# Kernel tuning notes

Hardware: AMD Instinct MI355X
Metric: run time of the kernel (lower is better)

The kernel has to match this reference:

```python
import jax, jax.numpy as jnp
import numpy as np

K_SIZE = 5


def _extract_patches(x, k):
    """x: [n, b, h, w, c] -> [n, b, h, w, k*k, c] with zero SAME padding.

    Matches tf.image.extract_patches row-major patch ordering with channels
    fastest, as consumed by the Reshape((H, W, k*k, Ci)) in the original.
    """
    p = k // 2
    n, b, h, w, c = x.shape
    xp = jnp.pad(x, ((0, 0), (0, 0), (p, p), (p, p), (0, 0)))
    shifts = [xp[:, :, i:i + h, j:j + w, :] for i in range(k) for j in range(k)]
    return jnp.stack(shifts, axis=4)


def setup_inputs() -> dict:
    key = jax.random.key(0)
    k1, k2, k3, k4 = jax.random.split(key, 4)
    B, H, W, C = 4, 128, 128, 64
    heads, Ci = 4, 16  # intermediate_dim=64, head_num=4
    main = jax.random.normal(k1, (B, H, W, C), jnp.float32)
    ref = jax.random.normal(k2, (B, H, W, C), jnp.float32)
    he_std = np.sqrt(2.0 / C).astype(np.float32)  # he_normal, fan_in=C (1x1 conv)
    w_main = jax.random.normal(k3, (heads, C, Ci), jnp.float32) * he_std
    w_ref = jax.random.normal(k4, (heads, C, Ci), jnp.float32) * he_std
    return {"main": main, "ref": ref, "w_main": w_main, "w_ref": w_ref}


def reference(main, ref, w_main, w_ref):
    # per-head 1x1 convs (no bias): [n,b,h,w,d]
    q = jnp.einsum('bhwc,ncd->nbhwd', main, w_main)
    r = jnp.einsum('bhwc,ncd->nbhwd', ref, w_ref)
    patches = _extract_patches(r, K_SIZE)          # [n,b,h,w,k*k,d]
    attn = jnp.einsum('nbhwd,nbhwkd->nbhwk', q, patches)
    attn = jax.nn.softmax(attn, axis=-1)           # softmax over k*k neighbors
    return jnp.mean(attn, axis=0)                  # average over heads -> [b,h,w,k*k]
```

## Files before the change

kernel.cpp:

```cpp
#include <hip/hip_runtime.h>
#include <hip/hip_bf16.h>

typedef _Float16 f16;
typedef f16 f16x2 __attribute__((ext_vector_type(2)));
typedef f16 f16x4 __attribute__((ext_vector_type(4)));
typedef f16 f16x8 __attribute__((ext_vector_type(8)));
typedef float f32x4 __attribute__((ext_vector_type(4)));

constexpr int B_  = 4;
constexpr int H_  = 128;
constexpr int W_  = 128;
constexpr int C_  = 64;
constexpr int NH_ = 4;
constexpr int D_  = 16;
constexpr int KK_ = 25;

constexpr int TW_  = 8, TH_ = 8;
constexpr int HWID = 12, HHEI = 12;
constexpr int NPX  = HHEI * HWID;
constexpr int MOFF  = NPX * 64 * 2;
constexpr int MSOFF = 27648;
constexpr int SMEM  = 31744;
constexpr int PSTRIDE = KK_ + 2;
constexpr int PSLAB   = 64 * PSTRIDE;

#if __has_builtin(__builtin_amdgcn_fdot2)
#define FDOT2(a, b, c) __builtin_amdgcn_fdot2((a), (b), (c), false)
#else
#define FDOT2(a, b, c) fmaf((float)(a)[1], (float)(b)[1], fmaf((float)(a)[0], (float)(b)[0], (c)))
#endif

__device__ __forceinline__ int div12(int x) { return (x * 171) >> 11; }

__global__ __launch_bounds__(512, 8) void rl8mh8(
    const float* __restrict__ mainp, const float* __restrict__ refp,
    const float* __restrict__ wmain, const float* __restrict__ wref,
    float* __restrict__ out)
{
    __shared__ __align__(16) unsigned char smraw[SMEM];
    f16*    abuf  = (f16*)smraw;
    f16*    mabuf = (f16*)(smraw + MOFF);
    float*  xbuf  = (float*)smraw;
    float2* msbuf = (float2*)(smraw + MSOFF);

    const int tid = threadIdx.x;
    const int l   = tid & 63;
    const int wid = __builtin_amdgcn_readfirstlane(tid >> 6);
    const int n   = wid & 3;
    const int h   = wid >> 2;
    const int row = l & 15;
    const int kg  = l >> 4;

    const int bid = blockIdx.y * 16 + blockIdx.x;
    const int swz = (bid & 7) * 32 + (bid >> 3);
    const int x0 = (swz & 15) * TW_;
    const int y0 = (swz >> 4) * TH_;
    const int b  = blockIdx.z;
    const float* mainb = mainp + ((size_t)b * H_) * W_ * C_;
    const float* refb  = refp  + ((size_t)b * H_) * W_ * C_;

    for (int j = tid; j < NPX * 16; j += 512) {
        int hp = j >> 4, c4 = j & 15;
        int hy = div12(hp), hx = hp - hy * HWID;
        int gy = y0 + hy - 2, gx = x0 + hx - 2;
        float4 v = make_float4(0.f, 0.f, 0.f, 0.f);
        if ((unsigned)gy < (unsigned)H_ && (unsigned)gx < (unsigned)W_)
            v = *(const float4*)(refb + ((size_t)gy * W_ + gx) * C_ + c4 * 4);
        f16x4 h4 = {(f16)v.x, (f16)v.y, (f16)v.z, (f16)v.w};
        int off = hp * 64 + ((((c4 >> 1) ^ (hp & 7)) << 3) | ((c4 & 1) << 2));
        *(f16x4*)(abuf + off) = h4;
    }
    for (int j = tid; j < 64 * 16; j += 512) {
        int px = j >> 4, c4 = j & 15;
        int gy = y0 + (px >> 3), gx = x0 + (px & 7);
        float4 v = *(const float4*)(mainb + ((size_t)gy * W_ + gx) * C_ + c4 * 4);
        f16x4 h4 = {(f16)v.x, (f16)v.y, (f16)v.z, (f16)v.w};
        int off = px * 64 + ((((c4 >> 1) ^ (px & 7)) << 3) | ((c4 & 1) << 2));
        *(f16x4*)(mabuf + off) = h4;
    }
    __syncthreads();

    auto build_w = [&](const float* wsrc, f16x8* A) {
        const float* w = wsrc + n * C_ * D_;
        #pragma unroll
        for (int s = 0; s < 2; ++s) {
            union { f16x8 v; f16 e[8]; } u;
            #pragma unroll
            for (int i = 0; i < 8; ++i)
                u.e[i] = (f16)w[(s * 32 + kg * 8 + i) * D_ + row];
            A[s] = u.v;
        }
    };

    auto proj = [&](const f16* src, int t, const f16x8* A) -> f16x4 {
        int px = t * 16 + row;
        const f16* rp = src + px * 64;
        f16x8 B0 = *(const f16x8*)(rp + (((kg     ^ (px & 7)) << 3)));
        f16x8 B1 = *(const f16x8*)(rp + ((((kg+4) ^ (px & 7)) << 3)));
        f32x4 acc = {0.f, 0.f, 0.f, 0.f};
        acc = __builtin_amdgcn_mfma_f32_16x16x32_f16(A[0], B0, acc, 0, 0, 0);
        acc = __builtin_amdgcn_mfma_f32_16x16x32_f16(A[1], B1, acc, 0, 0, 0);
        return f16x4{(f16)acc[0], (f16)acc[1], (f16)acc[2], (f16)acc[3]};
    };
    f16x4 racc0, racc1, racc2, racc3, racc4, qacc0, qacc1;
    {
        f16x8 ar[2];
        build_w(wref, ar);
        if (h == 0) {
            racc0 = proj(abuf, 0, ar); racc1 = proj(abuf, 2, ar);
            racc2 = proj(abuf, 4, ar); racc3 = proj(abuf, 6, ar);
            racc4 = proj(abuf, 8, ar);
        } else {
            racc0 = proj(abuf, 1, ar); racc1 = proj(abuf, 3, ar);
            racc2 = proj(abuf, 5, ar); racc3 = proj(abuf, 7, ar);
        }
    }
    {
        f16x8 am[2];
        build_w(wmain, am);
        if (h == 0) { qacc0 = proj(mabuf, 0, am); qacc1 = proj(mabuf, 2, am); }
        else        { qacc0 = proj(mabuf, 1, am); qacc1 = proj(mabuf, 3, am); }
    }
    __syncthreads();

    auto wrout = [&](f16* dst, int t, f16x4 v) {
        int px = t * 16 + row;
        int c16 = (n << 1) | (kg >> 1);
        int off = px * 64 + (((c16 ^ (px & 7)) << 3) | ((kg & 1) << 2));
        *(f16x4*)(dst + off) = v;
    };
    if (h == 0) {
        wrout(abuf, 0, racc0); wrout(abuf, 2, racc1); wrout(abuf, 4, racc2);
        wrout(abuf, 6, racc3); wrout(abuf, 8, racc4);
        wrout(mabuf, 0, qacc0); wrout(mabuf, 2, qacc1);
    } else {
        wrout(abuf, 1, racc0); wrout(abuf, 3, racc1); wrout(abuf, 5, racc2);
        wrout(abuf, 7, racc3);
        wrout(mabuf, 1, qacc0); wrout(mabuf, 3, qacc1);
    }
    __syncthreads();

    const int py  = l >> 3;
    const int pxx = l & 7;
    f16x8 q0 = *(const f16x8*)(mabuf + l * 64 + ((((n << 1) | 0) ^ (l & 7)) << 3));
    f16x8 q1 = *(const f16x8*)(mabuf + l * 64 + ((((n << 1) | 1) ^ (l & 7)) << 3));
    const f16x2* q2a = (const f16x2*)&q0;
    const f16x2* q2b = (const f16x2*)&q1;

    float lg[13];
    auto do_lg = [&](int idx, int k) {
        int ky = k / 5, kx = k % 5;
        int np = (py + ky) * 12 + pxx + kx;
        const f16* rp = abuf + np * 64;
        f16x8 r0 = *(const f16x8*)(rp + ((((n << 1) | 0) ^ (np & 7)) << 3));
        f16x8 r1 = *(const f16x8*)(rp + ((((n << 1) | 1) ^ (np & 7)) << 3));
        const f16x2* r2a = (const f16x2*)&r0;
        const f16x2* r2b = (const f16x2*)&r1;
        float a = 0.f;
        #pragma unroll
        for (int j = 0; j < 4; ++j) a = FDOT2(q2a[j], r2a[j], a);
        #pragma unroll
        for (int j = 0; j < 4; ++j) a = FDOT2(q2b[j], r2b[j], a);
        lg[idx] = a;
    };
    if (h == 0) {
        do_lg(0,0);  do_lg(1,1);  do_lg(2,2);  do_lg(3,3);  do_lg(4,4);
        do_lg(5,5);  do_lg(6,6);  do_lg(7,7);  do_lg(8,8);  do_lg(9,9);
        do_lg(10,10); do_lg(11,11); do_lg(12,12);
    } else {
        do_lg(0,13); do_lg(1,14); do_lg(2,15); do_lg(3,16); do_lg(4,17);
        do_lg(5,18); do_lg(6,19); do_lg(7,20); do_lg(8,21); do_lg(9,22);
        do_lg(10,23); do_lg(11,24);
        lg[12] = -1e30f;
    }

    float mloc = lg[0];
    #pragma unroll
    for (int k = 1; k < 13; ++k) mloc = fmaxf(mloc, lg[k]);

    float s = 0.f;
    f16x2 pk[7];
    #pragma unroll
    for (int j = 0; j < 6; ++j) {
        float e0 = __expf(lg[2*j]   - mloc);
        float e1 = __expf(lg[2*j+1] - mloc);
        s += e0 + e1;
        pk[j] = f16x2{(f16)e0, (f16)e1};
    }
    {
        float e12 = __expf(lg[12] - mloc);
        s += e12;
        pk[6] = f16x2{(f16)e12, (f16)0.f};
    }
    msbuf[(h * 4 + n) * 64 + l] = make_float2(mloc, s);
    __syncthreads();
    float2 o = msbuf[((1 - h) * 4 + n) * 64 + l];
    float m    = fmaxf(mloc, o.x);
    float sc   = __expf(mloc - m);
    float osc  = __expf(o.x  - m);
    float inv  = sc / (s * sc + o.y * osc);

    {
        float* dst = &xbuf[n * PSLAB + l * PSTRIDE + h * 13];
        #pragma unroll
        for (int j = 0; j < 6; ++j) {
            dst[2*j]     = (float)pk[j][0] * inv;
            dst[2*j + 1] = (float)pk[j][1] * inv;
        }
        if (h == 0) dst[12] = (float)pk[6][0] * inv;
    }
    __syncthreads();

    for (int i = tid; i < TW_ * TH_ * KK_; i += 512) {
        int p2 = i / KK_;
        int k  = i - p2 * KK_;
        int off = p2 * PSTRIDE + k;
        float v = 0.25f * (xbuf[off] + xbuf[PSLAB + off] + xbuf[2 * PSLAB + off] + xbuf[3 * PSLAB + off]);
        out[(((size_t)b * H_ + (y0 + (p2 >> 3))) * W_ + (x0 + (p2 & 7))) * KK_ + k] = v;
    }
}

extern "C" void kernel_launch(void* const* d_in, const int* in_sizes, int n_in,
                              void* d_out, int out_size, void* d_ws, size_t ws_size,
                              hipStream_t stream) {
    const float* mainp = (const float*)d_in[0];
    const float* refp  = (const float*)d_in[1];
    const float* wmain = (const float*)d_in[2];
    const float* wref  = (const float*)d_in[3];
    float* outp = (float*)d_out;

    dim3 grid(W_ / TW_, H_ / TH_, B_);
    rl8mh8<<<grid, dim3(512), 0, stream>>>(mainp, refp, wmain, wref, outp);
}
```

Baseline: 18.88 us.

## Project queries straight from global memory and reduce heads via LDS atomics

The main-image tile is no longer staged through LDS. Each wave loads main pixels directly from global memory into MFMA operands and writes only the projected queries to a small dedicated buffer, with the weight fragments hoisted to the kernel start. The per-head probability slabs are replaced by one accumulator that the heads update with LDS float atomicAdd, removing the four-way sum in the output loop. This cuts LDS footprint and staging work, at the cost of atomic contention in LDS and less coalesced direct global loads.

```diff
diff --git a/kernel.cpp b/kernel.cpp
--- a/kernel.cpp
+++ b/kernel.cpp
@@ -18,11 +18,12 @@
 constexpr int TW_  = 8, TH_ = 8;
 constexpr int HWID = 12, HHEI = 12;
 constexpr int NPX  = HHEI * HWID;
-constexpr int MOFF  = NPX * 64 * 2;
-constexpr int MSOFF = 27648;
-constexpr int SMEM  = 31744;
-constexpr int PSTRIDE = KK_ + 2;
-constexpr int PSLAB   = 64 * PSTRIDE;
+constexpr int QSTR  = 20;
+constexpr int QOFF  = NPX * 64 * 2;
+constexpr int POFF  = QOFF + NH_ * 64 * QSTR * 2;
+constexpr int MSOFF = POFF + 64 * 27 * 4;
+constexpr int SMEM  = MSOFF + 4096;
+constexpr int PSTR  = 27;
 
 #if __has_builtin(__builtin_amdgcn_fdot2)
 #define FDOT2(a, b, c) __builtin_amdgcn_fdot2((a), (b), (c), false)
@@ -32,15 +33,15 @@
 
 __device__ __forceinline__ int div12(int x) { return (x * 171) >> 11; }
 
-__global__ __launch_bounds__(512, 8) void rl8mh8(
+__global__ __launch_bounds__(512, 8) void rl8mh10(
     const float* __restrict__ mainp, const float* __restrict__ refp,
     const float* __restrict__ wmain, const float* __restrict__ wref,
     float* __restrict__ out)
 {
     __shared__ __align__(16) unsigned char smraw[SMEM];
     f16*    abuf  = (f16*)smraw;
-    f16*    mabuf = (f16*)(smraw + MOFF);
-    float*  xbuf  = (float*)smraw;
+    f16*    qbuf  = (f16*)(smraw + QOFF);
+    float*  pbuf  = (float*)(smraw + POFF);
     float2* msbuf = (float2*)(smraw + MSOFF);
 
     const int tid = threadIdx.x;
@@ -58,6 +59,23 @@
     const int b  = blockIdx.z;
     const float* mainb = mainp + ((size_t)b * H_) * W_ * C_;
     const float* refb  = refp  + ((size_t)b * H_) * W_ * C_;
+
+    f16x8 am[2], ar[2];
+    {
+        const float* wm = wmain + n * C_ * D_;
+        const float* wr = wref  + n * C_ * D_;
+        #pragma unroll
+        for (int s = 0; s < 2; ++s) {
+            union { f16x8 v; f16 e[8]; } um, ur;
+            #pragma unroll
+            for (int i = 0; i < 8; ++i) {
+                int k = (s * 32 + kg * 8 + i) * D_ + row;
+                um.e[i] = (f16)wm[k];
+                ur.e[i] = (f16)wr[k];
+            }
+            am[s] = um.v; ar[s] = ur.v;
+        }
+    }
 
     for (int j = tid; j < NPX * 16; j += 512) {
         int hp = j >> 4, c4 = j & 15;
@@ -70,82 +88,76 @@
         int off = hp * 64 + ((((c4 >> 1) ^ (hp & 7)) << 3) | ((c4 & 1) << 2));
         *(f16x4*)(abuf + off) = h4;
     }
-    for (int j = tid; j < 64 * 16; j += 512) {
-        int px = j >> 4, c4 = j & 15;
-        int gy = y0 + (px >> 3), gx = x0 + (px & 7);
-        float4 v = *(const float4*)(mainb + ((size_t)gy * W_ + gx) * C_ + c4 * 4);
-        f16x4 h4 = {(f16)v.x, (f16)v.y, (f16)v.z, (f16)v.w};
-        int off = px * 64 + ((((c4 >> 1) ^ (px & 7)) << 3) | ((c4 & 1) << 2));
-        *(f16x4*)(mabuf + off) = h4;
-    }
-    __syncthreads();
-
-    auto build_w = [&](const float* wsrc, f16x8* A) {
-        const float* w = wsrc + n * C_ * D_;
-        #pragma unroll
-        for (int s = 0; s < 2; ++s) {
-            union { f16x8 v; f16 e[8]; } u;
+    if (tid < (64 * PSTR) / 4) ((f32x4*)pbuf)[tid] = f32x4{0.f, 0.f, 0.f, 0.f};
+
+    {
+        #pragma unroll
+        for (int ti = 0; ti < 2; ++ti) {
+            int t  = ti * 2 + h;
+            int px = t * 16 + row;
+            int gy = y0 + (px >> 3), gx = x0 + (px & 7);
+            const float* src = mainb + ((size_t)gy * W_ + gx) * C_ + kg * 8;
+            f32x4 acc = {0.f, 0.f, 0.f, 0.f};
             #pragma unroll
-            for (int i = 0; i < 8; ++i)
-                u.e[i] = (f16)w[(s * 32 + kg * 8 + i) * D_ + row];
-            A[s] = u.v;
+            for (int s = 0; s < 2; ++s) {
+                float4 v0 = *(const float4*)(src + s * 32);
+                float4 v1 = *(const float4*)(src + s * 32 + 4);
+                union { f16x8 v; f16 e[8]; } u;
+                u.e[0]=(f16)v0.x; u.e[1]=(f16)v0.y; u.e[2]=(f16)v0.z; u.e[3]=(f16)v0.w;
+                u.e[4]=(f16)v1.x; u.e[5]=(f16)v1.y; u.e[6]=(f16)v1.z; u.e[7]=(f16)v1.w;
+                acc = __builtin_amdgcn_mfma_f32_16x16x32_f16(am[s], u.v, acc, 0, 0, 0);
+            }
+            f16x4 q4 = {(f16)acc[0], (f16)acc[1], (f16)acc[2], (f16)acc[3]};
+            *(f16x4*)(qbuf + (n * 64 + px) * QSTR + kg * 4) = q4;
         }
-    };
-
-    auto proj = [&](const f16* src, int t, const f16x8* A) -> f16x4 {
+    }
+    __syncthreads();
+
+    auto proj_r = [&](int t) -> f16x4 {
         int px = t * 16 + row;
-        const f16* rp = src + px * 64;
+        const f16* rp = abuf + px * 64;
         f16x8 B0 = *(const f16x8*)(rp + (((kg     ^ (px & 7)) << 3)));
         f16x8 B1 = *(const f16x8*)(rp + ((((kg+4) ^ (px & 7)) << 3)));
         f32x4 acc = {0.f, 0.f, 0.f, 0.f};
-        acc = __builtin_amdgcn_mfma_f32_16x16x32_f16(A[0], B0, acc, 0, 0, 0);
-        acc = __builtin_amdgcn_mfma_f32_16x16x32_f16(A[1], B1, acc, 0, 0, 0);
+        acc = __builtin_amdgcn_mfma_f32_16x16x32_f16(ar[0], B0, acc, 0, 0, 0);
+        acc = __builtin_amdgcn_mfma_f32_16x16x32_f16(ar[1], B1, acc, 0, 0, 0);
         return f16x4{(f16)acc[0], (f16)acc[1], (f16)acc[2], (f16)acc[3]};
     };
-    f16x4 racc0, racc1, racc2, racc3, racc4, qacc0, qacc1;
-    {
-        f16x8 ar[2];
-        build_w(wref, ar);
-        if (h == 0) {
-            racc0 = proj(abuf, 0, ar); racc1 = proj(abuf, 2, ar);
-            racc2 = proj(abuf, 4, ar); racc3 = proj(abuf, 6, ar);
-            racc4 = proj(abuf, 8, ar);
-        } else {
-            racc0 = proj(abuf, 1, ar); racc1 = proj(abuf, 3, ar);
-            racc2 = proj(abuf, 5, ar); racc3 = proj(abuf, 7, ar);
-        }
-    }
-    {
-        f16x8 am[2];
-        build_w(wmain, am);
-        if (h == 0) { qacc0 = proj(mabuf, 0, am); qacc1 = proj(mabuf, 2, am); }
-        else        { qacc0 = proj(mabuf, 1, am); qacc1 = proj(mabuf, 3, am); }
-    }
-    __syncthreads();
-
-    auto wrout = [&](f16* dst, int t, f16x4 v) {
+    f16x4 racc0, racc1, racc2, racc3, racc4;
+    if (h == 0) {
+        racc0 = proj_r(0); racc1 = proj_r(2); racc2 = proj_r(4);
+        racc3 = proj_r(6); racc4 = proj_r(8);
+    } else {
+        racc0 = proj_r(1); racc1 = proj_r(3); racc2 = proj_r(5);
+        racc3 = proj_r(7);
+    }
+    __syncthreads();
+
+    auto wrout = [&](int t, f16x4 v) {
         int px = t * 16 + row;
         int c16 = (n << 1) | (kg >> 1);
         int off = px * 64 + (((c16 ^ (px & 7)) << 3) | ((kg & 1) << 2));
-        *(f16x4*)(dst + off) = v;
+        *(f16x4*)(abuf + off) = v;
     };
     if (h == 0) {
-        wrout(abuf, 0, racc0); wrout(abuf, 2, racc1); wrout(abuf, 4, racc2);
-        wrout(abuf, 6, racc3); wrout(abuf, 8, racc4);
-        wrout(mabuf, 0, qacc0); wrout(mabuf, 2, qacc1);
+        wrout(0, racc0); wrout(2, racc1); wrout(4, racc2);
+        wrout(6, racc3); wrout(8, racc4);
     } else {
-        wrout(abuf, 1, racc0); wrout(abuf, 3, racc1); wrout(abuf, 5, racc2);
-        wrout(abuf, 7, racc3);
-        wrout(mabuf, 1, qacc0); wrout(mabuf, 3, qacc1);
+        wrout(1, racc0); wrout(3, racc1); wrout(5, racc2); wrout(7, racc3);
     }
     __syncthreads();
 
     const int py  = l >> 3;
     const int pxx = l & 7;
-    f16x8 q0 = *(const f16x8*)(mabuf + l * 64 + ((((n << 1) | 0) ^ (l & 7)) << 3));
-    f16x8 q1 = *(const f16x8*)(mabuf + l * 64 + ((((n << 1) | 1) ^ (l & 7)) << 3));
-    const f16x2* q2a = (const f16x2*)&q0;
-    const f16x2* q2b = (const f16x2*)&q1;
+    union { f16x4 v4[4]; f16x2 v2[8]; } qu;
+    {
+        const f16* qp = qbuf + (n * 64 + l) * QSTR;
+        qu.v4[0] = *(const f16x4*)(qp);
+        qu.v4[1] = *(const f16x4*)(qp + 4);
+        qu.v4[2] = *(const f16x4*)(qp + 8);
+        qu.v4[3] = *(const f16x4*)(qp + 12);
+    }
+    const f16x2* q2 = qu.v2;
 
     float lg[13];
     auto do_lg = [&](int idx, int k) {
@@ -158,9 +170,9 @@
         const f16x2* r2b = (const f16x2*)&r1;
         float a = 0.f;
         #pragma unroll
-        for (int j = 0; j < 4; ++j) a = FDOT2(q2a[j], r2a[j], a);
-        #pragma unroll
-        for (int j = 0; j < 4; ++j) a = FDOT2(q2b[j], r2b[j], a);
+        for (int j = 0; j < 4; ++j) a = FDOT2(q2[j], r2a[j], a);
+        #pragma unroll
+        for (int j = 0; j < 4; ++j) a = FDOT2(q2[4 + j], r2b[j], a);
         lg[idx] = a;
     };
     if (h == 0) {
@@ -201,21 +213,20 @@
     float inv  = sc / (s * sc + o.y * osc);
 
     {
-        float* dst = &xbuf[n * PSLAB + l * PSTRIDE + h * 13];
+        float* dst = &pbuf[l * PSTR + h * 13];
         #pragma unroll
         for (int j = 0; j < 6; ++j) {
-            dst[2*j]     = (float)pk[j][0] * inv;
-            dst[2*j + 1] = (float)pk[j][1] * inv;
+            atomicAdd(&dst[2*j],     (float)pk[j][0] * inv);
+            atomicAdd(&dst[2*j + 1], (float)pk[j][1] * inv);
         }
-        if (h == 0) dst[12] = (float)pk[6][0] * inv;
+        if (h == 0) atomicAdd(&dst[12], (float)pk[6][0] * inv);
     }
     __syncthreads();
 
     for (int i = tid; i < TW_ * TH_ * KK_; i += 512) {
         int p2 = i / KK_;
         int k  = i - p2 * KK_;
-        int off = p2 * PSTRIDE + k;
-        float v = 0.25f * (xbuf[off] + xbuf[PSLAB + off] + xbuf[2 * PSLAB + off] + xbuf[3 * PSLAB + off]);
+        float v = 0.25f * pbuf[p2 * PSTR + k];
         out[(((size_t)b * H_ + (y0 + (p2 >> 3))) * W_ + (x0 + (p2 & 7))) * KK_ + k] = v;
     }
 }
@@ -230,5 +241,5 @@
     float* outp = (float*)d_out;
 
     dim3 grid(W_ / TW_, H_ / TH_, B_);
-    rl8mh8<<<grid, dim3(512), 0, stream>>>(mainp, refp, wmain, wref, outp);
+    rl8mh10<<<grid, dim3(512), 0, stream>>>(mainp, refp, wmain, wref, outp);
 }
```

Measured after the change: 52.54 us. 178% more time.

## Switch projections to 32x32x16 MFMA with head-pair/pixel-group wave split

Applied to the files above, without the earlier changes.

Replaces the per-head 16x16x32 MFMA projections with 32x32x16 MFMAs that compute two heads (32 output channels) over 32 pixels at once. Work is redistributed so wave pairs own pixel groups of the halo or the main tile instead of each wave projecting both. Staging loads are widened to 8 channels (two float4) per thread, with fixed unrolled iterations and no strided loop. The goal is fewer MFMA issues and less LDS traffic per projected value. The tradeoff is an imbalance: one group handles only 16 valid pixels in a padded 32-pixel tile, and the larger accumulator uses more registers.

```diff
diff --git a/kernel.cpp b/kernel.cpp
--- a/kernel.cpp
+++ b/kernel.cpp
@@ -6,6 +6,7 @@
 typedef f16 f16x4 __attribute__((ext_vector_type(4)));
 typedef f16 f16x8 __attribute__((ext_vector_type(8)));
 typedef float f32x4 __attribute__((ext_vector_type(4)));
+typedef float f32x16 __attribute__((ext_vector_type(16)));
 
 constexpr int B_  = 4;
 constexpr int H_  = 128;
@@ -32,7 +33,7 @@
 
 __device__ __forceinline__ int div12(int x) { return (x * 171) >> 11; }
 
-__global__ __launch_bounds__(512, 8) void rl8mh8(
+__global__ __launch_bounds__(512, 8) void rl8mh12(
     const float* __restrict__ mainp, const float* __restrict__ refp,
     const float* __restrict__ wmain, const float* __restrict__ wref,
     float* __restrict__ out)
@@ -48,8 +49,8 @@
     const int wid = __builtin_amdgcn_readfirstlane(tid >> 6);
     const int n   = wid & 3;
     const int h   = wid >> 2;
-    const int row = l & 15;
-    const int kg  = l >> 4;
+    const int p   = wid & 1;
+    const int g   = wid >> 1;
 
     const int bid = blockIdx.y * 16 + blockIdx.x;
     const int swz = (bid & 7) * 32 + (bid >> 3);
@@ -59,85 +60,86 @@
     const float* mainb = mainp + ((size_t)b * H_) * W_ * C_;
     const float* refb  = refp  + ((size_t)b * H_) * W_ * C_;
 
-    for (int j = tid; j < NPX * 16; j += 512) {
-        int hp = j >> 4, c4 = j & 15;
-        int hy = div12(hp), hx = hp - hy * HWID;
+    auto stage_halo = [&](int j) {
+        int px = j >> 3, pc = j & 7;
+        int hy = div12(px), hx = px - hy * HWID;
         int gy = y0 + hy - 2, gx = x0 + hx - 2;
-        float4 v = make_float4(0.f, 0.f, 0.f, 0.f);
-        if ((unsigned)gy < (unsigned)H_ && (unsigned)gx < (unsigned)W_)
-            v = *(const float4*)(refb + ((size_t)gy * W_ + gx) * C_ + c4 * 4);
-        f16x4 h4 = {(f16)v.x, (f16)v.y, (f16)v.z, (f16)v.w};
-        int off = hp * 64 + ((((c4 >> 1) ^ (hp & 7)) << 3) | ((c4 & 1) << 2));
-        *(f16x4*)(abuf + off) = h4;
-    }
-    for (int j = tid; j < 64 * 16; j += 512) {
-        int px = j >> 4, c4 = j & 15;
+        float4 va = make_float4(0.f,0.f,0.f,0.f), vb = va;
+        if ((unsigned)gy < (unsigned)H_ && (unsigned)gx < (unsigned)W_) {
+            const float4* src = (const float4*)(refb + ((size_t)gy * W_ + gx) * C_);
+            va = src[pc * 2]; vb = src[pc * 2 + 1];
+        }
+        f16x8 h8 = {(f16)va.x,(f16)va.y,(f16)va.z,(f16)va.w,
+                    (f16)vb.x,(f16)vb.y,(f16)vb.z,(f16)vb.w};
+        *(f16x8*)(abuf + px * 64 + ((pc ^ (px & 7)) << 3)) = h8;
+    };
+    stage_halo(tid);
+    stage_halo(tid + 512);
+    if (tid < 128) stage_halo(tid + 1024);
+    {
+        int px = tid >> 3, pc = tid & 7;
         int gy = y0 + (px >> 3), gx = x0 + (px & 7);
-        float4 v = *(const float4*)(mainb + ((size_t)gy * W_ + gx) * C_ + c4 * 4);
-        f16x4 h4 = {(f16)v.x, (f16)v.y, (f16)v.z, (f16)v.w};
-        int off = px * 64 + ((((c4 >> 1) ^ (px & 7)) << 3) | ((c4 & 1) << 2));
-        *(f16x4*)(mabuf + off) = h4;
-    }
-    __syncthreads();
-
-    auto build_w = [&](const float* wsrc, f16x8* A) {
-        const float* w = wsrc + n * C_ * D_;
-        #pragma unroll
-        for (int s = 0; s < 2; ++s) {
+        const float4* src = (const float4*)(mainb + ((size_t)gy * W_ + gx) * C_);
+        float4 va = src[pc * 2], vb = src[pc * 2 + 1];
+        f16x8 h8 = {(f16)va.x,(f16)va.y,(f16)va.z,(f16)va.w,
+                    (f16)vb.x,(f16)vb.y,(f16)vb.z,(f16)vb.w};
+        *(f16x8*)(mabuf + px * 64 + ((pc ^ (px & 7)) << 3)) = h8;
+    }
+    __syncthreads();
+
+    f16x8 A[4];
+    {
+        const float* wsrc = (g == 3) ? wmain : wref;
+        int rowA = l & 31;
+        const float* w = wsrc + (p * 2 + (rowA >> 4)) * C_ * D_ + (rowA & 15);
+        int kbase = (l >> 5) * 8;
+        #pragma unroll
+        for (int s = 0; s < 4; ++s) {
             union { f16x8 v; f16 e[8]; } u;
             #pragma unroll
             for (int i = 0; i < 8; ++i)
-                u.e[i] = (f16)w[(s * 32 + kg * 8 + i) * D_ + row];
+                u.e[i] = (f16)w[(s * 16 + kbase + i) * D_];
             A[s] = u.v;
         }
-    };
-
-    auto proj = [&](const f16* src, int t, const f16x8* A) -> f16x4 {
-        int px = t * 16 + row;
+    }
+
+    auto proj32 = [&](const f16* src, int pbase, f16x4* o) {
+        int px = pbase + (l & 31);
         const f16* rp = src + px * 64;
-        f16x8 B0 = *(const f16x8*)(rp + (((kg     ^ (px & 7)) << 3)));
-        f16x8 B1 = *(const f16x8*)(rp + ((((kg+4) ^ (px & 7)) << 3)));
-        f32x4 acc = {0.f, 0.f, 0.f, 0.f};
-        acc = __builtin_amdgcn_mfma_f32_16x16x32_f16(A[0], B0, acc, 0, 0, 0);
-        acc = __builtin_amdgcn_mfma_f32_16x16x32_f16(A[1], B1, acc, 0, 0, 0);
-        return f16x4{(f16)acc[0], (f16)acc[1], (f16)acc[2], (f16)acc[3]};
-    };
-    f16x4 racc0, racc1, racc2, racc3, racc4, qacc0, qacc1;
-    {
-        f16x8 ar[2];
-        build_w(wref, ar);
-        if (h == 0) {
-            racc0 = proj(abuf, 0, ar); racc1 = proj(abuf, 2, ar);
-            racc2 = proj(abuf, 4, ar); racc3 = proj(abuf, 6, ar);
-            racc4 = proj(abuf, 8, ar);
-        } else {
-            racc0 = proj(abuf, 1, ar); racc1 = proj(abuf, 3, ar);
-            racc2 = proj(abuf, 5, ar); racc3 = proj(abuf, 7, ar);
-        }
-    }
-    {
-        f16x8 am[2];
-        build_w(wmain, am);
-        if (h == 0) { qacc0 = proj(mabuf, 0, am); qacc1 = proj(mabuf, 2, am); }
-        else        { qacc0 = proj(mabuf, 1, am); qacc1 = proj(mabuf, 3, am); }
-    }
-    __syncthreads();
-
-    auto wrout = [&](f16* dst, int t, f16x4 v) {
-        int px = t * 16 + row;
-        int c16 = (n << 1) | (kg >> 1);
-        int off = px * 64 + (((c16 ^ (px & 7)) << 3) | ((kg & 1) << 2));
-        *(f16x4*)(dst + off) = v;
-    };
-    if (h == 0) {
-        wrout(abuf, 0, racc0); wrout(abuf, 2, racc1); wrout(abuf, 4, racc2);
-        wrout(abuf, 6, racc3); wrout(abuf, 8, racc4);
-        wrout(mabuf, 0, qacc0); wrout(mabuf, 2, qacc1);
-    } else {
-        wrout(abuf, 1, racc0); wrout(abuf, 3, racc1); wrout(abuf, 5, racc2);
-        wrout(abuf, 7, racc3);
-        wrout(mabuf, 1, qacc0); wrout(mabuf, 3, qacc1);
-    }
+        f32x16 acc = {};
+        #pragma unroll
+        for (int s = 0; s < 4; ++s) {
+            f16x8 Bv = *(const f16x8*)(rp + (((s * 2 + (l >> 5)) ^ (px & 7)) << 3));
+            acc = __builtin_amdgcn_mfma_f32_32x32x16_f16(A[s], Bv, acc, 0, 0, 0);
+        }
+        #pragma unroll
+        for (int cc = 0; cc < 4; ++cc)
+            o[cc] = f16x4{(f16)acc[4*cc], (f16)acc[4*cc+1],
+                          (f16)acc[4*cc+2], (f16)acc[4*cc+3]};
+    };
+    auto wrout32 = [&](f16* dst, int pbase, int nvalid, const f16x4* o) {
+        int px = pbase + (l & 31);
+        if ((l & 31) < nvalid) {
+            int hi = l >> 5;
+            #pragma unroll
+            for (int cc = 0; cc < 4; ++cc) {
+                int c = (p * 2 + (cc >> 1)) * 2 + (cc & 1);
+                *(f16x4*)(dst + px * 64 + (((c ^ (px & 7)) << 3) | (hi << 2))) = o[cc];
+            }
+        }
+    };
+
+    f16x4 oA[4], oB[4];
+    if      (g == 0) { proj32(abuf,   0, oA); proj32(abuf,  32, oB); }
+    else if (g == 1) { proj32(abuf,  64, oA); proj32(abuf,  96, oB); }
+    else if (g == 2) { proj32(abuf, 128, oA); }
+    else             { proj32(mabuf,  0, oA); proj32(mabuf, 32, oB); }
+    __syncthreads();
+
+    if      (g == 0) { wrout32(abuf,   0, 32, oA); wrout32(abuf,  32, 32, oB); }
+    else if (g == 1) { wrout32(abuf,  64, 32, oA); wrout32(abuf,  96, 32, oB); }
+    else if (g == 2) { wrout32(abuf, 128, 16, oA); }
+    else             { wrout32(mabuf,  0, 32, oA); wrout32(mabuf, 32, 32, oB); }
     __syncthreads();
 
     const int py  = l >> 3;
@@ -230,5 +232,5 @@
     float* outp = (float*)d_out;
 
     dim3 grid(W_ / TW_, H_ / TH_, B_);
-    rl8mh8<<<grid, dim3(512), 0, stream>>>(mainp, refp, wmain, wref, outp);
+    rl8mh12<<<grid, dim3(512), 0, stream>>>(mainp, refp, wmain, wref, outp);
 }
```

New measurement: 19.10 us. No clear change (+1.2%).

## Shrink tile to 8x4 with 256 threads and split neighbors within a wave

Applied to the files above, without the earlier changes.

Halves the spatial tile to 8x4 pixels and the block to 4 waves, one per head. Each wave now covers 32 pixels, with the two lane halves splitting the 25 neighbors 13/12 using an overlapping index. The softmax max/sum exchange moves from an LDS buffer and barrier to a cross-lane shuffle. This cuts shared memory per block and doubles the grid for more occupancy, at the cost of a larger halo fraction (8 of 12 rows loaded for 4 output rows) and more redundant ref-projection work.

```diff
diff --git a/kernel.cpp b/kernel.cpp
--- a/kernel.cpp
+++ b/kernel.cpp
@@ -15,14 +15,13 @@
 constexpr int D_  = 16;
 constexpr int KK_ = 25;
 
-constexpr int TW_  = 8, TH_ = 8;
-constexpr int HWID = 12, HHEI = 12;
+constexpr int TW_  = 8, TH_ = 4;
+constexpr int HWID = 12, HHEI = 8;
 constexpr int NPX  = HHEI * HWID;
-constexpr int MOFF  = NPX * 64 * 2;
-constexpr int MSOFF = 27648;
-constexpr int SMEM  = 31744;
+constexpr int MOFF = NPX * 64 * 2;
+constexpr int SMEM = MOFF + 32 * 64 * 2;
 constexpr int PSTRIDE = KK_ + 2;
-constexpr int PSLAB   = 64 * PSTRIDE;
+constexpr int PSLAB   = 32 * PSTRIDE;
 
 #if __has_builtin(__builtin_amdgcn_fdot2)
 #define FDOT2(a, b, c) __builtin_amdgcn_fdot2((a), (b), (c), false)
@@ -31,35 +30,35 @@
 #endif
 
 __device__ __forceinline__ int div12(int x) { return (x * 171) >> 11; }
-
-__global__ __launch_bounds__(512, 8) void rl8mh8(
+__device__ __forceinline__ int div5(int x)  { return (x * 205) >> 10; }
+
+__global__ __launch_bounds__(256, 8) void rl8mh14(
     const float* __restrict__ mainp, const float* __restrict__ refp,
     const float* __restrict__ wmain, const float* __restrict__ wref,
     float* __restrict__ out)
 {
     __shared__ __align__(16) unsigned char smraw[SMEM];
-    f16*    abuf  = (f16*)smraw;
-    f16*    mabuf = (f16*)(smraw + MOFF);
-    float*  xbuf  = (float*)smraw;
-    float2* msbuf = (float2*)(smraw + MSOFF);
+    f16*   abuf  = (f16*)smraw;
+    f16*   mabuf = (f16*)(smraw + MOFF);
+    float* xbuf  = (float*)smraw;
 
     const int tid = threadIdx.x;
     const int l   = tid & 63;
-    const int wid = __builtin_amdgcn_readfirstlane(tid >> 6);
-    const int n   = wid & 3;
-    const int h   = wid >> 2;
+    const int n   = __builtin_amdgcn_readfirstlane(tid >> 6);
     const int row = l & 15;
     const int kg  = l >> 4;
 
     const int bid = blockIdx.y * 16 + blockIdx.x;
-    const int swz = (bid & 7) * 32 + (bid >> 3);
+    const int swz = (bid & 7) * 64 + (bid >> 3);
     const int x0 = (swz & 15) * TW_;
     const int y0 = (swz >> 4) * TH_;
     const int b  = blockIdx.z;
     const float* mainb = mainp + ((size_t)b * H_) * W_ * C_;
     const float* refb  = refp  + ((size_t)b * H_) * W_ * C_;
 
-    for (int j = tid; j < NPX * 16; j += 512) {
+    #pragma unroll
+    for (int t = 0; t < 6; ++t) {
+        int j  = t * 256 + tid;
         int hp = j >> 4, c4 = j & 15;
         int hy = div12(hp), hx = hp - hy * HWID;
         int gy = y0 + hy - 2, gx = x0 + hx - 2;
@@ -67,16 +66,16 @@
         if ((unsigned)gy < (unsigned)H_ && (unsigned)gx < (unsigned)W_)
             v = *(const float4*)(refb + ((size_t)gy * W_ + gx) * C_ + c4 * 4);
         f16x4 h4 = {(f16)v.x, (f16)v.y, (f16)v.z, (f16)v.w};
-        int off = hp * 64 + ((((c4 >> 1) ^ (hp & 7)) << 3) | ((c4 & 1) << 2));
-        *(f16x4*)(abuf + off) = h4;
-    }
-    for (int j = tid; j < 64 * 16; j += 512) {
+        *(f16x4*)(abuf + hp * 64 + ((((c4 >> 1) ^ (hp & 7)) << 3) | ((c4 & 1) << 2))) = h4;
+    }
+    #pragma unroll
+    for (int t = 0; t < 2; ++t) {
+        int j  = t * 256 + tid;
         int px = j >> 4, c4 = j & 15;
         int gy = y0 + (px >> 3), gx = x0 + (px & 7);
         float4 v = *(const float4*)(mainb + ((size_t)gy * W_ + gx) * C_ + c4 * 4);
         f16x4 h4 = {(f16)v.x, (f16)v.y, (f16)v.z, (f16)v.w};
-        int off = px * 64 + ((((c4 >> 1) ^ (px & 7)) << 3) | ((c4 & 1) << 2));
-        *(f16x4*)(mabuf + off) = h4;
+        *(f16x4*)(mabuf + px * 64 + ((((c4 >> 1) ^ (px & 7)) << 3) | ((c4 & 1) << 2))) = h4;
     }
     __syncthreads();
 
@@ -102,54 +101,47 @@
         acc = __builtin_amdgcn_mfma_f32_16x16x32_f16(A[1], B1, acc, 0, 0, 0);
         return f16x4{(f16)acc[0], (f16)acc[1], (f16)acc[2], (f16)acc[3]};
     };
-    f16x4 racc0, racc1, racc2, racc3, racc4, qacc0, qacc1;
+    f16x4 o[8];
     {
         f16x8 ar[2];
         build_w(wref, ar);
-        if (h == 0) {
-            racc0 = proj(abuf, 0, ar); racc1 = proj(abuf, 2, ar);
-            racc2 = proj(abuf, 4, ar); racc3 = proj(abuf, 6, ar);
-            racc4 = proj(abuf, 8, ar);
-        } else {
-            racc0 = proj(abuf, 1, ar); racc1 = proj(abuf, 3, ar);
-            racc2 = proj(abuf, 5, ar); racc3 = proj(abuf, 7, ar);
-        }
+        #pragma unroll
+        for (int t = 0; t < 6; ++t) o[t] = proj(abuf, t, ar);
     }
     {
         f16x8 am[2];
         build_w(wmain, am);
-        if (h == 0) { qacc0 = proj(mabuf, 0, am); qacc1 = proj(mabuf, 2, am); }
-        else        { qacc0 = proj(mabuf, 1, am); qacc1 = proj(mabuf, 3, am); }
+        #pragma unroll
+        for (int t = 0; t < 2; ++t) o[6 + t] = proj(mabuf, t, am);
     }
     __syncthreads();
 
     auto wrout = [&](f16* dst, int t, f16x4 v) {
         int px = t * 16 + row;
         int c16 = (n << 1) | (kg >> 1);
-        int off = px * 64 + (((c16 ^ (px & 7)) << 3) | ((kg & 1) << 2));
-        *(f16x4*)(dst + off) = v;
+        *(f16x4*)(dst + px * 64 + (((c16 ^ (px & 7)) << 3) | ((kg & 1) << 2))) = v;
     };
-    if (h == 0) {
-        wrout(abuf, 0, racc0); wrout(abuf, 2, racc1); wrout(abuf, 4, racc2);
-        wrout(abuf, 6, racc3); wrout(abuf, 8, racc4);
-        wrout(mabuf, 0, qacc0); wrout(mabuf, 2, qacc1);
-    } else {
-        wrout(abuf, 1, racc0); wrout(abuf, 3, racc1); wrout(abuf, 5, racc2);
-        wrout(abuf, 7, racc3);
-        wrout(mabuf, 1, qacc0); wrout(mabuf, 3, qacc1);
-    }
-    __syncthreads();
-
-    const int py  = l >> 3;
-    const int pxx = l & 7;
-    f16x8 q0 = *(const f16x8*)(mabuf + l * 64 + ((((n << 1) | 0) ^ (l & 7)) << 3));
-    f16x8 q1 = *(const f16x8*)(mabuf + l * 64 + ((((n << 1) | 1) ^ (l & 7)) << 3));
+    #pragma unroll
+    for (int t = 0; t < 6; ++t) wrout(abuf, t, o[t]);
+    #pragma unroll
+    for (int t = 0; t < 2; ++t) wrout(mabuf, t, o[6 + t]);
+    __syncthreads();
+
+    const int px  = l & 31;
+    const int h   = l >> 5;
+    const int py  = px >> 3;
+    const int pxx = px & 7;
+    f16x8 q0 = *(const f16x8*)(mabuf + px * 64 + ((((n << 1) | 0) ^ (px & 7)) << 3));
+    f16x8 q1 = *(const f16x8*)(mabuf + px * 64 + ((((n << 1) | 1) ^ (px & 7)) << 3));
     const f16x2* q2a = (const f16x2*)&q0;
     const f16x2* q2b = (const f16x2*)&q1;
 
     float lg[13];
-    auto do_lg = [&](int idx, int k) {
-        int ky = k / 5, kx = k % 5;
+    #pragma unroll
+    for (int j = 0; j < 13; ++j) {
+        int k  = h * 12 + j;
+        int ky = div5(k);
+        int kx = k - 5 * ky;
         int np = (py + ky) * 12 + pxx + kx;
         const f16* rp = abuf + np * 64;
         f16x8 r0 = *(const f16x8*)(rp + ((((n << 1) | 0) ^ (np & 7)) << 3));
@@ -158,60 +150,36 @@
         const f16x2* r2b = (const f16x2*)&r1;
         float a = 0.f;
         #pragma unroll
-        for (int j = 0; j < 4; ++j) a = FDOT2(q2a[j], r2a[j], a);
-        #pragma unroll
-        for (int j = 0; j < 4; ++j) a = FDOT2(q2b[j], r2b[j], a);
-        lg[idx] = a;
-    };
-    if (h == 0) {
-        do_lg(0,0);  do_lg(1,1);  do_lg(2,2);  do_lg(3,3);  do_lg(4,4);
-        do_lg(5,5);  do_lg(6,6);  do_lg(7,7);  do_lg(8,8);  do_lg(9,9);
-        do_lg(10,10); do_lg(11,11); do_lg(12,12);
-    } else {
-        do_lg(0,13); do_lg(1,14); do_lg(2,15); do_lg(3,16); do_lg(4,17);
-        do_lg(5,18); do_lg(6,19); do_lg(7,20); do_lg(8,21); do_lg(9,22);
-        do_lg(10,23); do_lg(11,24);
-        lg[12] = -1e30f;
+        for (int jj = 0; jj < 4; ++jj) a = FDOT2(q2a[jj], r2a[jj], a);
+        #pragma unroll
+        for (int jj = 0; jj < 4; ++jj) a = FDOT2(q2b[jj], r2b[jj], a);
+        lg[j] = a;
     }
 
     float mloc = lg[0];
     #pragma unroll
-    for (int k = 1; k < 13; ++k) mloc = fmaxf(mloc, lg[k]);
-
+    for (int j = 1; j < 13; ++j) mloc = fmaxf(mloc, lg[j]);
     float s = 0.f;
-    f16x2 pk[7];
-    #pragma unroll
-    for (int j = 0; j < 6; ++j) {
-        float e0 = __expf(lg[2*j]   - mloc);
-        float e1 = __expf(lg[2*j+1] - mloc);
-        s += e0 + e1;
-        pk[j] = f16x2{(f16)e0, (f16)e1};
-    }
+    #pragma unroll
+    for (int j = 0; j < 13; ++j) { lg[j] = __expf(lg[j] - mloc); s += lg[j]; }
+    float s_own = h ? (s - lg[0]) : s;
+    float om = __shfl_xor(mloc, 32);
+    float os = __shfl_xor(s_own, 32);
+    float m   = fmaxf(mloc, om);
+    float sc  = __expf(mloc - m);
+    float osc = __expf(om - m);
+    float inv = sc / (s_own * sc + os * osc);
+
+    __syncthreads();
+
     {
-        float e12 = __expf(lg[12] - mloc);
-        s += e12;
-        pk[6] = f16x2{(f16)e12, (f16)0.f};
-    }
-    msbuf[(h * 4 + n) * 64 + l] = make_float2(mloc, s);
-    __syncthreads();
-    float2 o = msbuf[((1 - h) * 4 + n) * 64 + l];
-    float m    = fmaxf(mloc, o.x);
-    float sc   = __expf(mloc - m);
-    float osc  = __expf(o.x  - m);
-    float inv  = sc / (s * sc + o.y * osc);
-
-    {
-        float* dst = &xbuf[n * PSLAB + l * PSTRIDE + h * 13];
-        #pragma unroll
-        for (int j = 0; j < 6; ++j) {
-            dst[2*j]     = (float)pk[j][0] * inv;
-            dst[2*j + 1] = (float)pk[j][1] * inv;
-        }
-        if (h == 0) dst[12] = (float)pk[6][0] * inv;
-    }
-    __syncthreads();
-
-    for (int i = tid; i < TW_ * TH_ * KK_; i += 512) {
+        float* dst = &xbuf[n * PSLAB + px * PSTRIDE + h * 12];
+        #pragma unroll
+        for (int j = 0; j < 13; ++j) dst[j] = lg[j] * inv;
+    }
+    __syncthreads();
+
+    for (int i = tid; i < TW_ * TH_ * KK_; i += 256) {
         int p2 = i / KK_;
         int k  = i - p2 * KK_;
         int off = p2 * PSTRIDE + k;
@@ -230,5 +198,5 @@
     float* outp = (float*)d_out;
 
     dim3 grid(W_ / TW_, H_ / TH_, B_);
-    rl8mh8<<<grid, dim3(512), 0, stream>>>(mainp, refp, wmain, wref, outp);
+    rl8mh14<<<grid, dim3(256), 0, stream>>>(mainp, refp, wmain, wref, outp);
 }
```

Result: slower. 25.02 us (+32.5%).
